# Kernel tuning notes

Hardware: AMD Instinct MI355X
Metric: run time of the kernel (lower is better)

The kernel has to match this reference:

```python
import jax, jax.numpy as jnp
import numpy as np

N_NODES = 50000
N_EDGES = 800000
N_GRAPHS = 64
NEG_SLOPE = 0.2  # PyG GATConv default leaky_relu slope
EPS = 1e-16      # PyG softmax denominator epsilon


def gat_conv(x, W, a_src, a_dst, bias, src, dst, n_nodes):
    """PyG GATConv (heads=1, concat=True, self-loops already appended).
    x: [N, F_in], W: [F_in, H*F], a_src/a_dst: [H, F], bias: [H*F]."""
    H, F = a_src.shape
    h = (x @ W).reshape(-1, H, F)                      # [N, H, F]
    alpha_src = jnp.einsum('nhf,hf->nh', h, a_src)     # [N, H]
    alpha_dst = jnp.einsum('nhf,hf->nh', h, a_dst)     # [N, H]
    e = jax.nn.leaky_relu(alpha_src[src] + alpha_dst[dst], NEG_SLOPE)  # [E, H]
    # segment softmax over incoming edges of each destination node
    e_max = jax.ops.segment_max(e, dst, num_segments=n_nodes)          # [N, H]
    e_exp = jnp.exp(e - e_max[dst])
    denom = jax.ops.segment_sum(e_exp, dst, num_segments=n_nodes)      # [N, H]
    alpha = e_exp / (denom[dst] + EPS)                                 # [E, H]
    msg = alpha[:, :, None] * h[src]                                   # [E, H, F]
    out = jax.ops.segment_sum(msg, dst, num_segments=n_nodes)          # [N, H, F]
    return out.reshape(-1, H * F) + bias


def global_mean_pool(x, batch, n_graphs):
    s = jax.ops.segment_sum(x, batch, num_segments=n_graphs)
    cnt = jax.ops.segment_sum(jnp.ones((x.shape[0],), x.dtype), batch, num_segments=n_graphs)
    return s / jnp.maximum(cnt, 1.0)[:, None]


def setup_inputs() -> dict:
    key = jax.random.key(0)
    ks = jax.random.split(key, 10)
    d_in, d_h, d_out, L, H = 128, 128, 10, 3, 1
    x = jax.random.normal(ks[0], (N_NODES, d_in), dtype=jnp.float32)
    edge_index = jax.random.randint(ks[1], (2, N_EDGES), 0, N_NODES, dtype=jnp.int32)
    edge_attr = jax.random.normal(ks[2], (N_EDGES, 4), dtype=jnp.float32)
    batch = jnp.sort(jax.random.randint(ks[3], (N_NODES,), 0, N_GRAPHS, dtype=jnp.int32))
    s0 = 1.0 / np.sqrt(d_in)
    sh = 1.0 / np.sqrt(d_h)
    return {
        'x': x,
        'edge_index': edge_index,
        'edge_attr': edge_attr,
        'batch': batch,
        'W0': jax.random.normal(ks[4], (d_in, d_h), dtype=jnp.float32) * s0,
        'b0': jnp.zeros((d_h,), jnp.float32),
        'Wc': jax.random.normal(ks[5], (L, d_h, H * d_h), dtype=jnp.float32) * sh,
        'att_src': jax.random.normal(ks[6], (L, H, d_h), dtype=jnp.float32) * sh,
        'att_dst': jax.random.normal(ks[7], (L, H, d_h), dtype=jnp.float32) * sh,
        'bc': jnp.zeros((L, H * d_h), jnp.float32),
        'W1': jax.random.normal(ks[8], (d_h, d_out), dtype=jnp.float32) * sh,
        'b1': jnp.zeros((d_out,), jnp.float32),
    }


def reference(x, edge_index, edge_attr, batch, W0, b0, Wc, att_src, att_dst, bc, W1, b1):
    n = x.shape[0]
    # GATConv default add_self_loops=True
    loops = jnp.arange(n, dtype=edge_index.dtype)
    src = jnp.concatenate([edge_index[0], loops])
    dst = jnp.concatenate([edge_index[1], loops])
    # dropout p=0 / eval mode -> identity
    h = jax.nn.relu(x @ W0 + b0)
    for i in range(Wc.shape[0]):
        h = jax.nn.relu(gat_conv(h, Wc[i], att_src[i], att_dst[i], bc[i], src, dst, n))
    pooled = global_mean_pool(h, batch, N_GRAPHS)   # [B, d_h]
    return pooled @ W1 + b1                          # [B, d_out]
```

## Files before the change

kernel.cpp:

```cpp
#include <hip/hip_runtime.h>
#include <hip/hip_bf16.h>
#include <hip/hip_fp16.h>
#include <hip/hip_fp8.h>

#define NN 50000
#define NE 800000
#define NG 64
#define DH 128

#define SEG 64
#define GEMMB 512
#define GEMMW (GEMMB * 4)
#define CST 136
#define CSTB 136
#define SMEM_BYTES 17408
#define NPAIR (NN / 2)
#define WTB 256
#define INITB ((NN + 255) / 256)
#define SCATB ((NE + 511) / 512)

#if defined(__has_builtin)
# if __has_builtin(__builtin_amdgcn_cvt_pk_f32_fp8) && __has_builtin(__builtin_amdgcn_cvt_pk_fp8_f32)
#  define HW_FP8 1
# endif
#endif

typedef __bf16 bfx8 __attribute__((ext_vector_type(8)));
typedef float  f32x4 __attribute__((ext_vector_type(4)));
typedef float  f32x8 __attribute__((ext_vector_type(8)));

__device__ __forceinline__ ushort f2b(float f) {
    unsigned b = __float_as_uint(f);
    b += 0x7fff + ((b >> 16) & 1);
    return (ushort)(b >> 16);
}
__device__ __forceinline__ float b2f(ushort s) {
    return __uint_as_float((unsigned)s << 16);
}
__device__ __forceinline__ unsigned pk2(float a, float b) {
    return (unsigned)f2b(a) | ((unsigned)f2b(b) << 16);
}

__device__ __forceinline__ unsigned f2fp8(float v) {
    v = fminf(fmaxf(v, -448.f), 448.f);
#ifdef HW_FP8
    return (unsigned)__builtin_amdgcn_cvt_pk_fp8_f32(v, v, 0, false) & 0xFFu;
#else
    __hip_fp8_e4m3 t(v);
    return (unsigned)*(const unsigned char*)&t;
#endif
}
__device__ __forceinline__ void fp8x4_up(unsigned u, float* o) {
#ifdef HW_FP8
    auto lo = __builtin_amdgcn_cvt_pk_f32_fp8((int)u, false);
    auto hi = __builtin_amdgcn_cvt_pk_f32_fp8((int)u, true);
    o[0] = lo[0]; o[1] = lo[1]; o[2] = hi[0]; o[3] = hi[1];
#else
    #pragma unroll
    for (int k = 0; k < 4; ++k) {
        unsigned char c = (u >> (8 * k)) & 0xFF;
        o[k] = float(*(const __hip_fp8_e4m3*)&c);
    }
#endif
}

__launch_bounds__(256)
__global__ void k_misc(const float* __restrict__ W0, const float* __restrict__ Wc,
                       ushort* __restrict__ Wt, int* __restrict__ cur,
                       ushort* __restrict__ csr) {
    int t = threadIdx.x;
    if (blockIdx.x < WTB) {
        int i = blockIdx.x * 256 + t;
        int m = i >> 14;
        int r = i & 16383;
        int k = r >> 7, n = r & 127;
        const float* src = (m == 0) ? W0 : (Wc + (size_t)(m - 1) * DH * DH);
        Wt[(size_t)m * DH * DH + n * DH + k] = f2b(src[r]);
        return;
    }
    int n = (blockIdx.x - WTB) * 256 + t;
    if (n < NN) {
        cur[n] = (n << 6) + 1;
        csr[(size_t)n << 6] = (ushort)n;
    }
}

__launch_bounds__(256)
__global__ void k_scatter(const int* __restrict__ ei, int* __restrict__ cur,
                          ushort* __restrict__ csr) {
    int e = blockIdx.x * 512 + threadIdx.x;
    #pragma unroll
    for (int j = 0; j < 2; ++j, e += 256) {
        if (e < NE) {
            int s = ei[e], d = ei[NE + e];
            int slot = atomicAdd(&cur[d], 1);
            if (slot < (d << 6) + SEG) csr[slot] = (ushort)s;
        }
    }
}

template<bool AF32, bool DOTS, bool OUTFP8>
__device__ __forceinline__ void gemm_body(char* smem, int gblk,
        const void* __restrict__ Av, const ushort* __restrict__ Wt,
        const float* __restrict__ bias, void* __restrict__ C, int relu,
        const float* __restrict__ avs, const float* __restrict__ avd,
        float* __restrict__ asrc, float* __restrict__ adst) {
    const int NT = NN / 16;
    int tid = threadIdx.x;
    int lane = tid & 63;
    int mrow = lane & 15;
    int quad = lane >> 4;
    int wid = (gblk * 256 + tid) >> 6;

    bfx8 b[4][8];
    #pragma unroll
    for (int ks = 0; ks < 4; ++ks) {
        int k0 = ks * 32 + quad * 8;
        #pragma unroll
        for (int t = 0; t < 8; ++t)
            b[ks][t] = *(const bfx8*)(Wt + (size_t)(t * 16 + mrow) * DH + k0);
    }
    float av[8], dv[8];
    if (DOTS) {
        #pragma unroll
        for (int t = 0; t < 8; ++t) {
            av[t] = avs[t * 16 + mrow];
            dv[t] = avd[t * 16 + mrow];
        }
    }

    for (int tile = wid; tile < NT; tile += GEMMW) {
        int row0 = tile * 16;
        int arow = row0 + mrow;

        bfx8 a[4];
        if (AF32) {
            f32x8 af[4];
            #pragma unroll
            for (int ks = 0; ks < 4; ++ks)
                af[ks] = *(const f32x8*)((const float*)Av + (size_t)arow * DH + ks * 32 + quad * 8);
            #pragma unroll
            for (int ks = 0; ks < 4; ++ks) {
                union { ushort s[8]; bfx8 v; } u;
                #pragma unroll
                for (int j = 0; j < 8; ++j) u.s[j] = f2b(af[ks][j]);
                a[ks] = u.v;
            }
        } else {
            #pragma unroll
            for (int ks = 0; ks < 4; ++ks)
                a[ks] = *(const bfx8*)((const ushort*)Av + (size_t)arow * DH + ks * 32 + quad * 8);
        }

        f32x4 acc[8];
        #pragma unroll
        for (int t = 0; t < 8; ++t)
            #pragma unroll
            for (int r = 0; r < 4; ++r) acc[t][r] = 0.f;

        #pragma unroll
        for (int ks = 0; ks < 4; ++ks)
            #pragma unroll
            for (int t = 0; t < 8; ++t)
                acc[t] = __builtin_amdgcn_mfma_f32_16x16x32_bf16(a[ks], b[ks][t], acc[t], 0, 0, 0);

        if (OUTFP8) {
            uchar* my = (uchar*)smem + (tid >> 6) * 16 * CSTB;
            #pragma unroll
            for (int t = 0; t < 8; ++t) {
                int col = t * 16 + mrow;
                float bv = bias ? bias[col] : 0.f;
                #pragma unroll
                for (int r = 0; r < 4; ++r) {
                    float v = acc[t][r] + bv;
                    if (relu) v = fmaxf(v, 0.f);
                    my[(quad * 4 + r) * CSTB + col] = (uchar)f2fp8(v);
                }
            }
            #pragma unroll
            for (int i = 0; i < 4; ++i) {
                int idx = i * 64 + lane;
                int row = idx >> 4;
                int c8 = idx & 15;
                uint2 u = *(const uint2*)(my + row * CSTB + c8 * 8);
                *(uint2*)((uchar*)C + (size_t)(row0 + row) * DH + c8 * 8) = u;
            }
        } else {
            ushort* my = (ushort*)smem + (tid >> 6) * 16 * CST;
            #pragma unroll
            for (int t = 0; t < 8; ++t) {
                int col = t * 16 + mrow;
                float bv = bias ? bias[col] : 0.f;
                #pragma unroll
                for (int r = 0; r < 4; ++r) {
                    float v = acc[t][r] + bv;
                    if (relu) v = fmaxf(v, 0.f);
                    my[(quad * 4 + r) * CST + col] = f2b(v);
                }
            }
            #pragma unroll
            for (int i = 0; i < 4; ++i) {
                int idx = i * 64 + lane;
                int row = idx >> 4;
                int c16 = idx & 15;
                uint4 u = *(const uint4*)(my + row * CST + c16 * 8);
                *(uint4*)((ushort*)C + (size_t)(row0 + row) * DH + c16 * 8) = u;
            }
        }

        if (DOTS) {
            int orow = row0 + quad * 4;
            #pragma unroll
            for (int r = 0; r < 4; ++r) {
                float ps = 0.f, pd = 0.f;
                #pragma unroll
                for (int t = 0; t < 8; ++t) {
                    ps += acc[t][r] * av[t];
                    pd += acc[t][r] * dv[t];
                }
                #pragma unroll
                for (int off = 1; off < 16; off <<= 1) {
                    ps += __shfl_xor(ps, off);
                    pd += __shfl_xor(pd, off);
                }
                if (mrow == 0) {
                    asrc[orow + r] = ps;
                    adst[orow + r] = pd;
                }
            }
        }
    }
}

__launch_bounds__(256)
__global__ void k_gemm1(const float* __restrict__ x, const ushort* __restrict__ Wt,
                        const float* __restrict__ b0, ushort* __restrict__ hB) {
    __shared__ char smem[SMEM_BYTES];
    gemm_body<true, false, false>(smem, blockIdx.x, x, Wt, b0, hB, 1,
                                  nullptr, nullptr, nullptr, nullptr);
}

__launch_bounds__(256)
__global__ void k_gemmdots(const ushort* __restrict__ hB, const ushort* __restrict__ Wt,
                           uchar* __restrict__ hA,
                           const float* __restrict__ avs, const float* __restrict__ avd,
                           float* __restrict__ asrc, float* __restrict__ adst) {
    __shared__ char smem[SMEM_BYTES];
    gemm_body<false, true, true>(smem, blockIdx.x, hB, Wt, nullptr, hA, 0,
                                 avs, avd, asrc, adst);
}

__device__ __forceinline__ void aggr_one(int wid, int lane,
        const uchar* __restrict__ h8, const float* __restrict__ asrc,
        const float* __restrict__ adst, const int* __restrict__ cur,
        const ushort* __restrict__ csr,
        const float* __restrict__ bias, ushort* __restrict__ hout) {
    int start = wid << 6;
    int cnt = min(cur[wid] - start, SEG);
    float ad = adst[wid];

    int s = csr[start + lane];
    float e = -1e30f;
    if (lane < cnt) {
        float t = asrc[s] + ad;
        e = fmaxf(t, 0.f) + 0.2f * fminf(t, 0.f);
    }
    float m = e;
    #pragma unroll
    for (int off = 32; off; off >>= 1) m = fmaxf(m, __shfl_xor(m, off));
    float w = (lane < cnt) ? __expf(e - m) : 0.f;
    float dsum = w;
    #pragma unroll
    for (int off = 32; off; off >>= 1) dsum += __shfl_xor(dsum, off);

    int g = lane >> 4, fidx = lane & 15;
    float acc[8];
    #pragma unroll
    for (int k = 0; k < 8; ++k) acc[k] = 0.f;

    int steps = (cnt + 3) >> 2;
    const uint2* hp = (const uint2*)h8;
    for (int j = 0; j < steps; ++j) {
        int e0 = j * 4 + g;
        float w0 = __shfl(w, e0);
        int   s0 = __shfl(s, e0);
        uint2 u0 = hp[(size_t)s0 * 16 + fidx];
        float v[8];
        fp8x4_up(u0.x, v); fp8x4_up(u0.y, v + 4);
        #pragma unroll
        for (int k = 0; k < 8; ++k) acc[k] += w0 * v[k];
    }
    #pragma unroll
    for (int k = 0; k < 8; ++k) {
        acc[k] += __shfl_xor(acc[k], 16);
        acc[k] += __shfl_xor(acc[k], 32);
    }
    if (g == 0) {
        float inv = 1.f / (dsum + 1e-16f);
        const float4* bp = (const float4*)bias;
        float4 b0 = bp[fidx * 2], b1 = bp[fidx * 2 + 1];
        uint4 o;
        o.x = pk2(fmaxf(acc[0] * inv + b0.x, 0.f), fmaxf(acc[1] * inv + b0.y, 0.f));
        o.y = pk2(fmaxf(acc[2] * inv + b0.z, 0.f), fmaxf(acc[3] * inv + b0.w, 0.f));
        o.z = pk2(fmaxf(acc[4] * inv + b1.x, 0.f), fmaxf(acc[5] * inv + b1.y, 0.f));
        o.w = pk2(fmaxf(acc[6] * inv + b1.z, 0.f), fmaxf(acc[7] * inv + b1.w, 0.f));
        ((uint4*)hout)[(size_t)wid * 16 + fidx] = o;
    }
}

__launch_bounds__(256)
__global__ void k_aggr(const uchar* __restrict__ h8, const float* __restrict__ asrc,
                       const float* __restrict__ adst, const int* __restrict__ cur,
                       const ushort* __restrict__ csr,
                       const float* __restrict__ bias, ushort* __restrict__ hout) {
    int pid = (blockIdx.x * blockDim.x + threadIdx.x) >> 6;
    int lane = threadIdx.x & 63;
    if (pid >= NPAIR) return;
    int half = lane >> 5, hl = lane & 31;
    int nd = pid * 2 + half;
    int start = nd << 6;

    int cnt = min(cur[nd] - start, SEG);
    int cother = __shfl_xor(cnt, 32);
    if (max(cnt, cother) <= 32) {
        float ad = adst[nd];
        int s = csr[start + hl];
        float e = -1e30f;
        if (hl < cnt) {
            float t = asrc[s] + ad;
            e = fmaxf(t, 0.f) + 0.2f * fminf(t, 0.f);
        }
        float m = e;
        #pragma unroll
        for (int off = 16; off; off >>= 1) m = fmaxf(m, __shfl_xor(m, off));
        float w = (hl < cnt) ? __expf(e - m) : 0.f;
        float dsum = w;
        #pragma unroll
        for (int off = 16; off; off >>= 1) dsum += __shfl_xor(dsum, off);

        int g = hl >> 4, fidx = hl & 15;
        int lbase = half * 32;
        float acc[8];
        #pragma unroll
        for (int k = 0; k < 8; ++k) acc[k] = 0.f;

        int steps = (cnt + 1) >> 1;
        const uint2* hp = (const uint2*)h8;
        int j = 0;
        for (; j + 3 < steps; j += 4) {
            int   e0 = j * 2 + g,       e1 = e0 + 2, e2 = e0 + 4, e3 = e0 + 6;
            float w0 = __shfl(w, lbase + e0), w1 = __shfl(w, lbase + e1);
            float w2 = __shfl(w, lbase + e2), w3 = __shfl(w, lbase + e3);
            int   s0 = __shfl(s, lbase + e0), s1 = __shfl(s, lbase + e1);
            int   s2 = __shfl(s, lbase + e2), s3 = __shfl(s, lbase + e3);
            uint2 u0 = hp[(size_t)s0 * 16 + fidx];
            uint2 u1 = hp[(size_t)s1 * 16 + fidx];
            uint2 u2 = hp[(size_t)s2 * 16 + fidx];
            uint2 u3 = hp[(size_t)s3 * 16 + fidx];
            float v[8];
            fp8x4_up(u0.x, v); fp8x4_up(u0.y, v + 4);
            #pragma unroll
            for (int k = 0; k < 8; ++k) acc[k] += w0 * v[k];
            fp8x4_up(u1.x, v); fp8x4_up(u1.y, v + 4);
            #pragma unroll
            for (int k = 0; k < 8; ++k) acc[k] += w1 * v[k];
            fp8x4_up(u2.x, v); fp8x4_up(u2.y, v + 4);
            #pragma unroll
            for (int k = 0; k < 8; ++k) acc[k] += w2 * v[k];
            fp8x4_up(u3.x, v); fp8x4_up(u3.y, v + 4);
            #pragma unroll
            for (int k = 0; k < 8; ++k) acc[k] += w3 * v[k];
        }
        for (; j < steps; ++j) {
            int   e0 = j * 2 + g;
            float w0 = __shfl(w, lbase + e0);
            int   s0 = __shfl(s, lbase + e0);
            uint2 u0 = hp[(size_t)s0 * 16 + fidx];
            float v[8];
            fp8x4_up(u0.x, v); fp8x4_up(u0.y, v + 4);
            #pragma unroll
            for (int k = 0; k < 8; ++k) acc[k] += w0 * v[k];
        }
        #pragma unroll
        for (int k = 0; k < 8; ++k) acc[k] += __shfl_xor(acc[k], 16);
        if (g == 0) {
            float inv = 1.f / (dsum + 1e-16f);
            const float4* bp = (const float4*)bias;
            float4 b0 = bp[fidx * 2], b1 = bp[fidx * 2 + 1];
            uint4 o;
            o.x = pk2(fmaxf(acc[0] * inv + b0.x, 0.f), fmaxf(acc[1] * inv + b0.y, 0.f));
            o.y = pk2(fmaxf(acc[2] * inv + b0.z, 0.f), fmaxf(acc[3] * inv + b0.w, 0.f));
            o.z = pk2(fmaxf(acc[4] * inv + b1.x, 0.f), fmaxf(acc[5] * inv + b1.y, 0.f));
            o.w = pk2(fmaxf(acc[6] * inv + b1.z, 0.f), fmaxf(acc[7] * inv + b1.w, 0.f));
            ((uint4*)hout)[(size_t)nd * 16 + fidx] = o;
        }
        return;
    }

    aggr_one(pid * 2,     lane, h8, asrc, adst, cur, csr, bias, hout);
    aggr_one(pid * 2 + 1, lane, h8, asrc, adst, cur, csr, bias, hout);
}

__launch_bounds__(256)
__global__ void k_pool(const ushort* __restrict__ h, const int* __restrict__ batch,
                       float* __restrict__ gsum, int* __restrict__ gcnt) {
    int slot = threadIdx.x >> 7;
    int f = threadIdx.x & 127;
    int n0 = blockIdx.x * 64;
    int n1 = min(n0 + 64, NN);
    int first = n0 + slot;
    if (first >= n1) return;
    int g0 = batch[n0], g1 = batch[n1 - 1];
    if (g0 == g1) {
        float acc = 0.f;
        for (int nd = first; nd < n1; nd += 2)
            acc += b2f(h[(size_t)nd * DH + f]);
        atomicAdd(&gsum[g0 * DH + f], acc);
        if (f == 0 && slot == 0) atomicAdd(&gcnt[g0], n1 - n0);
        return;
    }
    float acc = 0.f; int run = 0;
    int gcur = batch[first];
    for (int nd = first; nd < n1; nd += 2) {
        int g = batch[nd];
        if (g != gcur) {
            atomicAdd(&gsum[gcur * DH + f], acc);
            if (f == 0) atomicAdd(&gcnt[gcur], run);
            acc = 0.f; run = 0; gcur = g;
        }
        acc += b2f(h[(size_t)nd * DH + f]);
        run += 1;
    }
    atomicAdd(&gsum[gcur * DH + f], acc);
    if (f == 0) atomicAdd(&gcnt[gcur], run);
}

__global__ void k_final(const float* __restrict__ gsum, const int* __restrict__ gcnt,
                        const float* __restrict__ W1, const float* __restrict__ b1,
                        float* __restrict__ out) {
    int t = threadIdx.x;
    if (t >= NG * 10) return;
    int g = t / 10, o = t % 10;
    float inv = 1.f / fmaxf((float)gcnt[g], 1.f);
    float acc = 0.f;
    for (int f = 0; f < DH; ++f) acc += gsum[g * DH + f] * W1[f * 10 + o];
    out[t] = acc * inv + b1[o];
}

extern "C" void kernel_launch(void* const* d_in, const int* in_sizes, int n_in,
                              void* d_out, int out_size, void* d_ws, size_t ws_size,
                              hipStream_t stream) {
    const float* x       = (const float*)d_in[0];
    const int*   ei      = (const int*)d_in[1];
    const int*   batch   = (const int*)d_in[3];
    const float* W0      = (const float*)d_in[4];
    const float* b0      = (const float*)d_in[5];
    const float* Wc      = (const float*)d_in[6];
    const float* att_src = (const float*)d_in[7];
    const float* att_dst = (const float*)d_in[8];
    const float* bc      = (const float*)d_in[9];
    const float* W1      = (const float*)d_in[10];
    const float* b1      = (const float*)d_in[11];
    float* out = (float*)d_out;

    char* ws = (char*)d_ws;
    size_t off = 0;
    auto alloc = [&](size_t bytes) {
        void* p = ws + off;
        off += (bytes + 255) & ~(size_t)255;
        return p;
    };
    uchar*    hA     = (uchar*)alloc((size_t)NN * DH);
    ushort*   hB     = (ushort*)alloc((size_t)NN * DH * 2);
    ushort*   Wt     = (ushort*)alloc((size_t)4 * DH * DH * 2);
    ushort*   csr    = (ushort*)alloc((size_t)NN * SEG * 2);
    int*      cur    = (int*)alloc((size_t)NN * 4);
    float*    asrc   = (float*)alloc(NN * 4);
    float*    adst   = (float*)alloc(NN * 4);
    float*    gsum   = (float*)alloc(NG * DH * 4);
    int*      gcnt   = (int*)alloc(NG * 4);

    hipMemsetAsync(csr, 0, (size_t)NN * SEG * 2, stream);
    hipMemsetAsync(gsum, 0, NG * DH * 4 + 256, stream);

    k_misc<<<WTB + INITB, 256, 0, stream>>>(W0, Wc, Wt, cur, csr);
    k_scatter<<<SCATB, 256, 0, stream>>>(ei, cur, csr);
    k_gemm1<<<GEMMB, 256, 0, stream>>>(x, Wt, b0, hB);

    for (int l = 0; l < 3; ++l) {
        k_gemmdots<<<GEMMB, 256, 0, stream>>>(hB, Wt + (size_t)(l + 1) * DH * DH, hA,
                                              att_src + l * DH, att_dst + l * DH,
                                              asrc, adst);
        k_aggr<<<(NPAIR + 3) / 4, 256, 0, stream>>>(hA, asrc, adst, cur, csr,
                                                    bc + l * DH, hB);
    }

    k_pool<<<(NN + 63) / 64, 256, 0, stream>>>(hB, batch, gsum, gcnt);
    k_final<<<1, NG * 10, 0, stream>>>(gsum, gcnt, W1, b1, out);
}
```

Baseline: 321.3 us.

## Fuse CSR scatter into prep kernel with XCD-partitioned destination ranges

The separate init and scatter kernels are merged into one prep kernel. Each edge chunk is now read by 8 blocks, and each block handles only destinations inside one eighth of the node range, presumably so the atomics and CSR writes for a given node range stay in one XCD's L2. The per-node cursor becomes a zero-based count cleared by the extended memset instead of an init kernel. In exchange, the destination indices are read eight times over and most loads are filtered out.

```diff
diff --git a/kernel.cpp b/kernel.cpp
--- a/kernel.cpp
+++ b/kernel.cpp
@@ -15,11 +15,18 @@
 #define CSTB 136
 #define SMEM_BYTES 17408
 #define NPAIR (NN / 2)
+#define NXCD 8
+#define XNODES (NN / NXCD)
+#define CHUNKE 4096
+#define NCHUNK ((NE + CHUNKE - 1) / CHUNKE)
+#define SCATB (NCHUNK * NXCD)
 #define WTB 256
 #define INITB ((NN + 255) / 256)
-#define SCATB ((NE + 511) / 512)
+#define PREPB (SCATB + WTB + INITB)
 
 #if defined(__has_builtin)
+# if __has_builtin(__builtin_amdgcn_cvt_pk_f32_fp8) && __has_builtin(__builtin_amdgcn_cvt_pk_f32_fp8)
+# endif
 # if __has_builtin(__builtin_amdgcn_cvt_pk_f32_fp8) && __has_builtin(__builtin_amdgcn_cvt_pk_fp8_f32)
 #  define HW_FP8 1
 # endif
@@ -65,12 +72,38 @@
 }
 
 __launch_bounds__(256)
-__global__ void k_misc(const float* __restrict__ W0, const float* __restrict__ Wc,
-                       ushort* __restrict__ Wt, int* __restrict__ cur,
-                       ushort* __restrict__ csr) {
+__global__ void k_prep(const int* __restrict__ ei, int* __restrict__ cur,
+                       ushort* __restrict__ csr,
+                       const float* __restrict__ W0, const float* __restrict__ Wc,
+                       ushort* __restrict__ Wt) {
     int t = threadIdx.x;
-    if (blockIdx.x < WTB) {
-        int i = blockIdx.x * 256 + t;
+    unsigned bid = blockIdx.x;
+    if (bid < SCATB) {
+        int chunk = bid >> 3;
+        int lo = (int)(bid & 7) * XNODES;
+        int base = chunk * CHUNKE + t;
+        #pragma unroll
+        for (int jj = 0; jj < 16; jj += 4) {
+            int dd[4], ee[4];
+            #pragma unroll
+            for (int q = 0; q < 4; ++q) {
+                ee[q] = base + (jj + q) * 256;
+                dd[q] = (ee[q] < NE) ? ei[NE + ee[q]] : -1;
+            }
+            #pragma unroll
+            for (int q = 0; q < 4; ++q) {
+                if ((unsigned)(dd[q] - lo) < (unsigned)XNODES) {
+                    int s = ei[ee[q]];
+                    int slot = atomicAdd(&cur[dd[q]], 1);
+                    if (slot < SEG - 1)
+                        csr[((size_t)dd[q] << 6) + 1 + slot] = (ushort)s;
+                }
+            }
+        }
+        return;
+    }
+    if (bid < SCATB + WTB) {
+        int i = (bid - SCATB) * 256 + t;
         int m = i >> 14;
         int r = i & 16383;
         int k = r >> 7, n = r & 127;
@@ -78,25 +111,8 @@
         Wt[(size_t)m * DH * DH + n * DH + k] = f2b(src[r]);
         return;
     }
-    int n = (blockIdx.x - WTB) * 256 + t;
-    if (n < NN) {
-        cur[n] = (n << 6) + 1;
-        csr[(size_t)n << 6] = (ushort)n;
-    }
-}
-
-__launch_bounds__(256)
-__global__ void k_scatter(const int* __restrict__ ei, int* __restrict__ cur,
-                          ushort* __restrict__ csr) {
-    int e = blockIdx.x * 512 + threadIdx.x;
-    #pragma unroll
-    for (int j = 0; j < 2; ++j, e += 256) {
-        if (e < NE) {
-            int s = ei[e], d = ei[NE + e];
-            int slot = atomicAdd(&cur[d], 1);
-            if (slot < (d << 6) + SEG) csr[slot] = (ushort)s;
-        }
-    }
+    int n = (bid - SCATB - WTB) * 256 + t;
+    if (n < NN) csr[(size_t)n << 6] = (ushort)n;
 }
 
 template<bool AF32, bool DOTS, bool OUTFP8>
@@ -256,7 +272,7 @@
         const ushort* __restrict__ csr,
         const float* __restrict__ bias, ushort* __restrict__ hout) {
     int start = wid << 6;
-    int cnt = min(cur[wid] - start, SEG);
+    int cnt = min(cur[wid] + 1, SEG);
     float ad = adst[wid];
 
     int s = csr[start + lane];
@@ -320,7 +336,7 @@
     int nd = pid * 2 + half;
     int start = nd << 6;
 
-    int cnt = min(cur[nd] - start, SEG);
+    int cnt = min(cur[nd] + 1, SEG);
     int cother = __shfl_xor(cnt, 32);
     if (max(cnt, cother) <= 32) {
         float ad = adst[nd];
@@ -480,11 +496,10 @@
     float*    gsum   = (float*)alloc(NG * DH * 4);
     int*      gcnt   = (int*)alloc(NG * 4);
 
-    hipMemsetAsync(csr, 0, (size_t)NN * SEG * 2, stream);
+    hipMemsetAsync(csr, 0, (size_t)NN * SEG * 2 + (size_t)NN * 4, stream);
     hipMemsetAsync(gsum, 0, NG * DH * 4 + 256, stream);
 
-    k_misc<<<WTB + INITB, 256, 0, stream>>>(W0, Wc, Wt, cur, csr);
-    k_scatter<<<SCATB, 256, 0, stream>>>(ei, cur, csr);
+    k_prep<<<PREPB, 256, 0, stream>>>(ei, cur, csr, W0, Wc, Wt);
     k_gemm1<<<GEMMB, 256, 0, stream>>>(x, Wt, b0, hB);
 
     for (int l = 0; l < 3; ++l) {
```

New measurement: 302.0 us. 6.0% less time.
